# Kernel tuning notes

Measured on AMD Instinct MI355X. Metric: run time of the kernel, lower is better.

Reference implementation:

```python
import jax, jax.numpy as jnp
import numpy as np

EPS = 1e-5


def sage_conv(x, src, dst, Wl, Wr, b, n):
    # PyG SAGEConv: out_i = W_l * mean_{j in N(i)} x_j + W_r * x_i + b
    agg = jax.ops.segment_sum(x[src], dst, num_segments=n)  # [N, d]
    deg = jax.ops.segment_sum(jnp.ones_like(src, dtype=x.dtype), dst, num_segments=n)
    agg = agg / jnp.maximum(deg, 1.0)[:, None]
    return agg @ Wl + x @ Wr + b


def setup_inputs() -> dict:
    key = jax.random.key(0)
    ks = jax.random.split(key, 12)
    N, E, D_IN, D_H, D_OUT = 50000, 600000, 128, 128, 64
    x = jax.random.normal(ks[0], (N, D_IN), dtype=jnp.float32)
    edge_index = jax.random.randint(ks[1], (2, E), 0, N, dtype=jnp.int64)
    s_in = 1.0 / np.sqrt(D_IN)
    s_h = 1.0 / np.sqrt(D_H)
    return {
        "x": x,
        "edge_index": edge_index,
        "Wl0": jax.random.normal(ks[2], (D_IN, D_H), jnp.float32) * s_in,
        "Wr0": jax.random.normal(ks[3], (D_IN, D_H), jnp.float32) * s_in,
        "b0": jnp.zeros((D_H,), jnp.float32),
        "Wl1": jax.random.normal(ks[4], (D_H, D_H), jnp.float32) * s_h,
        "Wr1": jax.random.normal(ks[5], (D_H, D_H), jnp.float32) * s_h,
        "b1": jnp.zeros((D_H,), jnp.float32),
        "Wl2": jax.random.normal(ks[6], (D_H, D_OUT), jnp.float32) * s_h,
        "Wr2": jax.random.normal(ks[7], (D_H, D_OUT), jnp.float32) * s_h,
        "b2": jnp.zeros((D_OUT,), jnp.float32),
        "gamma": jnp.ones((D_H,), jnp.float32),
        "beta": jnp.zeros((D_H,), jnp.float32),
    }


def reference(x, edge_index, Wl0, Wr0, b0, Wl1, Wr1, b1, Wl2, Wr2, b2, gamma, beta):
    n = x.shape[0]
    src, dst = edge_index[0], edge_index[1]
    residual = x  # in_channels == hidden_channels -> no residual_transform
    # layer 0: conv + relu (+ dropout as identity in eval)
    h = jax.nn.relu(sage_conv(x, src, dst, Wl0, Wr0, b0, n))
    # middle layer: conv + BN(batch stats) + relu + residual
    h = sage_conv(h, src, dst, Wl1, Wr1, b1, n)
    mu = jnp.mean(h, axis=0)
    var = jnp.var(h, axis=0)  # biased, as in torch BN normalization
    h = (h - mu) * jax.lax.rsqrt(var + EPS) * gamma + beta
    h = jax.nn.relu(h) + residual
    # output layer
    h = sage_conv(h, src, dst, Wl2, Wr2, b2, n)
    return jax.nn.log_softmax(h, axis=-1)
```

## Files before the change

### kernel.cpp

```cpp
#include <hip/hip_runtime.h>
#include <hip/hip_bf16.h>


#define WS_EPS 1e-5f

typedef unsigned short ushort_t;
typedef unsigned int uint_t;
typedef unsigned char uchar_t;
typedef ushort_t ushort8 __attribute__((ext_vector_type(8)));
typedef short short8 __attribute__((ext_vector_type(8)));
typedef float f32x4 __attribute__((ext_vector_type(4)));
typedef _Float16 half2v __attribute__((ext_vector_type(2)));

__device__ __forceinline__ float bf2f(ushort_t u) {
    return __uint_as_float(((uint_t)u) << 16);
}
__device__ __forceinline__ ushort_t f2bf(float f) {
    uint_t u = __float_as_uint(f);
    u = (u + 0x7fffu + ((u >> 16) & 1u)) >> 16;
    return (ushort_t)u;
}
__device__ __forceinline__ uchar_t f2e4m3(float f) {
    _Float16 hf = (_Float16)f;
    uint_t h = (uint_t)__builtin_bit_cast(unsigned short, hf);
    uint_t s = (h >> 8) & 0x80u;
    uint_t r = h & 0x7fffu;
    if (r < 0x2400u) return (uchar_t)0;
    if (r > 0x5F40u) r = 0x5F00u;
    uint_t u = r - 0x2000u;
    uint_t m = (u + 0x3fu + ((u >> 7) & 1u)) >> 7;
    return (uchar_t)(s | m);
}

constexpr int SCHUNK = 4096;

__global__ __launch_bounds__(256) void k_scan_part(const int* __restrict__ deg,
                                                   int* __restrict__ bsum, int n) {
    int t = threadIdx.x;
    int base = blockIdx.x * SCHUNK + t * 16;
    int s = 0;
#pragma unroll
    for (int j = 0; j < 16; ++j) {
        int i = base + j;
        if (i < n) s += deg[i];
    }
#pragma unroll
    for (int d = 1; d < 64; d <<= 1) s += __shfl_xor(s, d);
    __shared__ int wt[4];
    if ((t & 63) == 0) wt[t >> 6] = s;
    __syncthreads();
    if (t == 0) bsum[blockIdx.x] = wt[0] + wt[1] + wt[2] + wt[3];
}

__global__ __launch_bounds__(64) void k_scan_bsum(const int* __restrict__ bsum,
                                                  int* __restrict__ boff,
                                                  int* __restrict__ off_n, int nb) {
    int lane = threadIdx.x;
    int carry = 0;
    for (int base = 0; base < nb; base += 64) {
        int t = base + lane;
        int v = (t < nb) ? bsum[t] : 0;
        int x = v;
#pragma unroll
        for (int d = 1; d < 64; d <<= 1) {
            int y = __shfl_up(x, d);
            if (lane >= d) x += y;
        }
        if (t < nb) boff[t] = carry + x - v;
        carry += __shfl(x, 63);
    }
    if (lane == 0) *off_n = carry;
}

__global__ __launch_bounds__(256) void k_scan_apply(const int* __restrict__ deg,
                                                    const int* __restrict__ boff,
                                                    int* __restrict__ off, int n) {
    int t = threadIdx.x;
    int lane = t & 63, wid = t >> 6;
    int base = blockIdx.x * SCHUNK + t * 16;
    int v[16];
    int s = 0;
#pragma unroll
    for (int j = 0; j < 16; ++j) {
        int i = base + j;
        v[j] = (i < n) ? deg[i] : 0;
        s += v[j];
    }
    int x = s;
#pragma unroll
    for (int d = 1; d < 64; d <<= 1) {
        int y = __shfl_up(x, d);
        if (lane >= d) x += y;
    }
    __shared__ int wtot[4];
    if (lane == 63) wtot[wid] = x;
    __syncthreads();
    int woff = 0;
    for (int wj = 0; wj < wid; ++wj) woff += wtot[wj];
    int run = boff[blockIdx.x] + woff + x - s;
#pragma unroll
    for (int j = 0; j < 16; ++j) {
        int i = base + j;
        if (i < n) off[i] = run;
        run += v[j];
    }
}

__global__ __launch_bounds__(256) void k_scatter(const int* __restrict__ ei,
                                                 const int* __restrict__ off,
                                                 int* __restrict__ cur,
                                                 int* __restrict__ csr, int E) {
    int e = blockIdx.x * 256 + threadIdx.x;
    if (e < E) {
        int d = ei[E + e];
        int s = ei[e];
        int p = atomicAdd(&cur[d], 1);
        csr[off[d] + p] = s;
    }
}

__global__ __launch_bounds__(256) void k_deg_prep(const int* __restrict__ ei,
                                                  int* __restrict__ deg, int E, int eb,
                                                  const float* __restrict__ x,
                                                  ushort_t* __restrict__ xb,
                                                  uchar_t* __restrict__ x8,
                                                  int total2, int nb_cvt,
                                                  const float* __restrict__ Wl0,
                                                  const float* __restrict__ Wr0,
                                                  const float* __restrict__ Wl1,
                                                  const float* __restrict__ Wr1,
                                                  const float* __restrict__ Wl2,
                                                  const float* __restrict__ Wr2,
                                                  ushort_t* __restrict__ wts) {
    int b = blockIdx.x;
    if (b < eb) {
        int e = b * 256 + threadIdx.x;
        if (e < E) atomicAdd(&deg[ei[E + e]], 1);
        return;
    }
    b -= eb;
    if (b < nb_cvt) {
        int i = b * 256 + threadIdx.x;
        if (i >= total2) return;
        float2 v = *(const float2*)&x[(size_t)i * 2];
        uint_t p = (uint_t)f2bf(v.x) | ((uint_t)f2bf(v.y) << 16);
        *(uint_t*)&xb[(size_t)i * 2] = p;
        ushort_t q = (ushort_t)((uint_t)f2e4m3(v.x) | ((uint_t)f2e4m3(v.y) << 8));
        *(ushort_t*)&x8[(size_t)i * 2] = q;
        return;
    }
    int id = (b - nb_cvt) * 256 + threadIdx.x;
    if (id >= 81920) return;
    const float* W;
    int rel, nout, base;
    if (id < 65536) {
        int m = id >> 14;
        rel = id & 16383;
        nout = 128;
        base = m << 14;
        W = (m == 0) ? Wl0 : (m == 1) ? Wr0 : (m == 2) ? Wl1 : Wr1;
    } else {
        int m = (id - 65536) >> 13;
        rel = (id - 65536) & 8191;
        nout = 64;
        base = 65536 + (m << 13);
        W = (m == 0) ? Wl2 : Wr2;
    }
    int c = rel >> 7;
    int k = rel & 127;
    wts[base + rel] = f2bf(W[(size_t)k * nout + c]);
}

template <int EPI>
__global__ __launch_bounds__(256, 4) void k_dgemm(const ushort_t* __restrict__ X1,
                                                  const ushort_t* __restrict__ W1,
                                                  const ushort_t* __restrict__ X2,
                                                  const ushort_t* __restrict__ W2,
                                                  const float* __restrict__ bias,
                                                  ushort_t* __restrict__ outp,
                                                  uchar_t* __restrict__ out8, int n) {
    constexpr int K = 128, NOUT = 128;
    __shared__ ushort_t Bs[2048 * 8];

    const int t = threadIdx.x;
    const int lane = t & 63;
    const int r16 = lane & 15, kb = lane >> 4;
    const int half = blockIdx.x & 1;
    const int colbase = half * 64;
    const int strip = (blockIdx.x >> 1) * 4 + (t >> 6);
    const int strips = (n + 15) >> 4;

    ushort8 wreg[8];
#pragma unroll
    for (int u = 0; u < 8; ++u) {
        int slot = u * 256 + t;
        int mat = slot >> 10;
        int rem = slot & 1023;
        int fnks = rem >> 6;
        int l = rem & 63;
        int fn = fnks >> 2, ks = fnks & 3;
        const ushort_t* Wm = mat ? W2 : W1;
        wreg[u] = *(const ushort8*)&Wm[(size_t)(colbase + fn * 16 + (l & 15)) * K +
                                       ks * 32 + (l >> 4) * 8];
    }
    const int arow = strip * 16 + r16;
    const bool rok = (arow < n);
    const size_t xo = (size_t)arow * K + kb * 8;
    short8 a1[4], a2[4];
#pragma unroll
    for (int ks = 0; ks < 4; ++ks)
        a1[ks] = rok ? *(const short8*)&X1[xo + ks * 32] : (short8)0;
#pragma unroll
    for (int ks = 0; ks < 4; ++ks)
        a2[ks] = rok ? *(const short8*)&X2[xo + ks * 32] : (short8)0;
#pragma unroll
    for (int u = 0; u < 8; ++u) {
        int slot = u * 256 + t;
        *(ushort8*)&Bs[(size_t)slot * 8] = wreg[u];
    }
    __syncthreads();

    f32x4 acc[4] = {(f32x4)0.f, (f32x4)0.f, (f32x4)0.f, (f32x4)0.f};
#pragma unroll
    for (int ks = 0; ks < 4; ++ks)
#pragma unroll
        for (int fn = 0; fn < 4; ++fn) {
            short8 b = *(const short8*)&Bs[((fn * 4 + ks) * 64 + lane) * 8];
            acc[fn] = __builtin_amdgcn_mfma_f32_16x16x32_bf16(a1[ks], b, acc[fn], 0, 0, 0);
        }
#pragma unroll
    for (int ks = 0; ks < 4; ++ks)
#pragma unroll
        for (int fn = 0; fn < 4; ++fn) {
            short8 b = *(const short8*)&Bs[((16 + fn * 4 + ks) * 64 + lane) * 8];
            acc[fn] = __builtin_amdgcn_mfma_f32_16x16x32_bf16(a2[ks], b, acc[fn], 0, 0, 0);
        }

    float bcol[4];
#pragma unroll
    for (int fn = 0; fn < 4; ++fn) bcol[fn] = bias[colbase + fn * 16 + r16];

    const int rb = strip * 16 + kb * 4;
#pragma unroll
    for (int r = 0; r < 4; ++r) {
        int row = rb + r;
        if (row >= n) continue;
#pragma unroll
        for (int fn = 0; fn < 4; ++fn) {
            int col = colbase + fn * 16 + r16;
            float v = acc[fn][r] + bcol[fn];
            if constexpr (EPI == 2) {
                v = fmaxf(v, 0.f);
                outp[(size_t)row * NOUT + col] = f2bf(v);
                out8[(size_t)row * NOUT + col] = f2e4m3(v);
            } else {
                outp[(size_t)row * NOUT + col] = f2bf(v);
            }
        }
    }
}

__global__ __launch_bounds__(256, 4) void k_cgemm(const ushort_t* __restrict__ H,
                                                  const ushort_t* __restrict__ WL,
                                                  const ushort_t* __restrict__ WR,
                                                  const float* __restrict__ b2,
                                                  ushort_t* __restrict__ A64,
                                                  ushort_t* __restrict__ Tb, int n) {
    constexpr int K = 128;
    __shared__ ushort_t Bs[2048 * 8];

    const int t = threadIdx.x;
    const int lane = t & 63;
    const int r16 = lane & 15, kb = lane >> 4;
    const int strip = blockIdx.x * 4 + (t >> 6);
    const int strips = (n + 15) >> 4;
    (void)strips;

    ushort8 wreg[8];
#pragma unroll
    for (int u = 0; u < 8; ++u) {
        int slot = u * 256 + t;
        int mat = slot >> 10;
        int rem = slot & 1023;
        int fnks = rem >> 6;
        int l = rem & 63;
        int fn = fnks >> 2, ks = fnks & 3;
        const ushort_t* Wm = mat ? WR : WL;
        wreg[u] = *(const ushort8*)&Wm[(size_t)(fn * 16 + (l & 15)) * K +
                                       ks * 32 + (l >> 4) * 8];
    }
    const int arow = strip * 16 + r16;
    const bool rok = (arow < n);
    const size_t xo = (size_t)arow * K + kb * 8;
    short8 a[4];
#pragma unroll
    for (int ks = 0; ks < 4; ++ks)
        a[ks] = rok ? *(const short8*)&H[xo + ks * 32] : (short8)0;
#pragma unroll
    for (int u = 0; u < 8; ++u) {
        int slot = u * 256 + t;
        *(ushort8*)&Bs[(size_t)slot * 8] = wreg[u];
    }
    __syncthreads();

    f32x4 aL[4] = {(f32x4)0.f, (f32x4)0.f, (f32x4)0.f, (f32x4)0.f};
    f32x4 aR[4] = {(f32x4)0.f, (f32x4)0.f, (f32x4)0.f, (f32x4)0.f};
#pragma unroll
    for (int ks = 0; ks < 4; ++ks)
#pragma unroll
        for (int fn = 0; fn < 4; ++fn) {
            short8 bl = *(const short8*)&Bs[((fn * 4 + ks) * 64 + lane) * 8];
            short8 br = *(const short8*)&Bs[((16 + fn * 4 + ks) * 64 + lane) * 8];
            aL[fn] = __builtin_amdgcn_mfma_f32_16x16x32_bf16(a[ks], bl, aL[fn], 0, 0, 0);
            aR[fn] = __builtin_amdgcn_mfma_f32_16x16x32_bf16(a[ks], br, aR[fn], 0, 0, 0);
        }

    float bcol[4];
#pragma unroll
    for (int fn = 0; fn < 4; ++fn) bcol[fn] = b2[fn * 16 + r16];

    const int rb = strip * 16 + kb * 4;
#pragma unroll
    for (int r = 0; r < 4; ++r) {
        int row = rb + r;
        if (row >= n) continue;
#pragma unroll
        for (int fn = 0; fn < 4; ++fn) {
            int col = fn * 16 + r16;
            A64[(size_t)row * 64 + col] = f2bf(aL[fn][r]);
            Tb[(size_t)row * 64 + col] = f2bf(aR[fn][r] + bcol[fn]);
        }
    }
}

__global__ __launch_bounds__(256) void k_bnstats(const ushort_t* __restrict__ P,
                                                 float* __restrict__ stats, int n) {
    int t = threadIdx.x;
    int c2 = t & 63;
    int h = t >> 6;
    int r0 = blockIdx.x * 64;
    int rend = min(r0 + 64, n);
    float s0 = 0.f, s1 = 0.f, q0 = 0.f, q1 = 0.f;
    for (int r = r0 + h; r < rend; r += 4) {
        uint_t pv = *(const uint_t*)&P[(size_t)r * 128 + c2 * 2];
        float p0 = __uint_as_float(pv << 16);
        float p1 = __uint_as_float(pv & 0xffff0000u);
        s0 += p0;
        q0 += p0 * p0;
        s1 += p1;
        q1 += p1 * p1;
    }
    __shared__ float sh[4][64][4];
    sh[h][c2][0] = s0;
    sh[h][c2][1] = s1;
    sh[h][c2][2] = q0;
    sh[h][c2][3] = q1;
    __syncthreads();
    if (h == 0) {
        float S0 = 0.f, S1 = 0.f, Q0 = 0.f, Q1 = 0.f;
#pragma unroll
        for (int j = 0; j < 4; ++j) {
            S0 += sh[j][c2][0];
            S1 += sh[j][c2][1];
            Q0 += sh[j][c2][2];
            Q1 += sh[j][c2][3];
        }
        atomicAdd(&stats[c2 * 2], S0);
        atomicAdd(&stats[c2 * 2 + 1], S1);
        atomicAdd(&stats[128 + c2 * 2], Q0);
        atomicAdd(&stats[128 + c2 * 2 + 1], Q1);
    }
}

__global__ __launch_bounds__(256) void k_segmean8(const uchar_t* __restrict__ U8,
                                                  const int* __restrict__ off,
                                                  const int* __restrict__ srcs,
                                                  ushort_t* __restrict__ out, int n) {
    int node = blockIdx.x * 32 + (threadIdx.x >> 3);
    int sub = threadIdx.x & 7;
    if (node >= n) return;
    int beg = off[node], end = off[node + 1];
    half2v aE0 = (half2v)0, aE1 = (half2v)0, aE2 = (half2v)0, aE3 = (half2v)0;
    half2v aO0 = (half2v)0, aO1 = (half2v)0, aO2 = (half2v)0, aO3 = (half2v)0;

#define DEC(dw, AE, AO)                                                           \
    {                                                                             \
        uint_t xe = (dw)&0x00ff00ffu;                                             \
        uint_t xo = ((dw) >> 8) & 0x00ff00ffu;                                    \
        uint_t he = ((xe & 0x00800080u) << 8) |                                   \
                    (((xe & 0x007f007fu) << 7) + 0x20002000u);                    \
        uint_t ho = ((xo & 0x00800080u) << 8) |                                   \
                    (((xo & 0x007f007fu) << 7) + 0x20002000u);                    \
        AE += __builtin_bit_cast(half2v, he);                                     \
        AO += __builtin_bit_cast(half2v, ho);                                     \
    }

    auto addrow = [&](int sidx) {
        uint4 v = *(const uint4*)&U8[(size_t)sidx * 128 + sub * 16];
        DEC(v.x, aE0, aO0)
        DEC(v.y, aE1, aO1)
        DEC(v.z, aE2, aO2)
        DEC(v.w, aE3, aO3)
    };
#undef DEC

    int i = beg;
    for (; i + 8 <= end; i += 8) {
        int sv[8];
#pragma unroll
        for (int u = 0; u < 8; ++u) sv[u] = srcs[i + u];
#pragma unroll
        for (int u = 0; u < 8; ++u) addrow(sv[u]);
    }
    for (; i < end; ++i) addrow(srcs[i]);

    int d = end - beg;
    float inv = 1.f / (float)(d > 1 ? d : 1);
    ushort8 o0, o1;
#define PACK(AE, AO, O, IDX)                     \
    O[IDX] = f2bf((float)AE[0] * inv);           \
    O[IDX + 1] = f2bf((float)AO[0] * inv);       \
    O[IDX + 2] = f2bf((float)AE[1] * inv);       \
    O[IDX + 3] = f2bf((float)AO[1] * inv);
    PACK(aE0, aO0, o0, 0)
    PACK(aE1, aO1, o0, 4)
    PACK(aE2, aO2, o1, 0)
    PACK(aE3, aO3, o1, 4)
#undef PACK
    *(ushort8*)&out[(size_t)node * 128 + sub * 16] = o0;
    *(ushort8*)&out[(size_t)node * 128 + sub * 16 + 8] = o1;
}

__global__ __launch_bounds__(256) void k_segmean_lsm(const ushort_t* __restrict__ A64,
                                                     const int* __restrict__ off,
                                                     const int* __restrict__ srcs,
                                                     const ushort_t* __restrict__ Tb,
                                                     float* __restrict__ out, int n) {
    int node = blockIdx.x * 32 + (threadIdx.x >> 3);
    int sub = threadIdx.x & 7;
    if (node >= n) return;
    int beg = off[node], end = off[node + 1];
    float a[8];
#pragma unroll
    for (int j = 0; j < 8; ++j) a[j] = 0.f;
    int i = beg;
    for (; i + 8 <= end; i += 8) {
        int sv[8];
#pragma unroll
        for (int u = 0; u < 8; ++u) sv[u] = srcs[i + u];
#pragma unroll
        for (int u = 0; u < 8; ++u) {
            ushort8 v = *(const ushort8*)&A64[(size_t)sv[u] * 64 + sub * 8];
#pragma unroll
            for (int j = 0; j < 8; ++j) a[j] += bf2f((ushort_t)v[j]);
        }
    }
    for (; i < end; ++i) {
        ushort8 v = *(const ushort8*)&A64[(size_t)srcs[i] * 64 + sub * 8];
#pragma unroll
        for (int j = 0; j < 8; ++j) a[j] += bf2f((ushort_t)v[j]);
    }
    int d = end - beg;
    float inv = 1.f / (float)(d > 1 ? d : 1);
    ushort8 tv = *(const ushort8*)&Tb[(size_t)node * 64 + sub * 8];
    float vv[8];
#pragma unroll
    for (int j = 0; j < 8; ++j) vv[j] = a[j] * inv + bf2f((ushort_t)tv[j]);
    float m = vv[0];
#pragma unroll
    for (int j = 1; j < 8; ++j) m = fmaxf(m, vv[j]);
#pragma unroll
    for (int dd = 1; dd < 8; dd <<= 1) m = fmaxf(m, __shfl_xor(m, dd));
    float e = 0.f;
#pragma unroll
    for (int j = 0; j < 8; ++j) e += expf(vv[j] - m);
#pragma unroll
    for (int dd = 1; dd < 8; dd <<= 1) e += __shfl_xor(e, dd);
    float lg = m + logf(e);
    f32x4 o0, o1;
#pragma unroll
    for (int j = 0; j < 4; ++j) {
        o0[j] = vv[j] - lg;
        o1[j] = vv[4 + j] - lg;
    }
    *(f32x4*)&out[(size_t)node * 64 + sub * 8] = o0;
    *(f32x4*)&out[(size_t)node * 64 + sub * 8 + 4] = o1;
}

__global__ __launch_bounds__(256) void k_bnapply(const ushort_t* __restrict__ P,
                                                 const ushort_t* __restrict__ Xb,
                                                 const float* __restrict__ stats,
                                                 const float* __restrict__ gamma,
                                                 const float* __restrict__ beta,
                                                 ushort_t* __restrict__ H, int n) {
    int i = blockIdx.x * 256 + threadIdx.x;
    if (i >= n * 64) return;
    int nd = i >> 6;
    int c = (i & 63) << 1;
    float inv_n = 1.f / (float)n;
    float mu0 = stats[c] * inv_n, mu1 = stats[c + 1] * inv_n;
    float v0 = stats[128 + c] * inv_n - mu0 * mu0;
    float v1 = stats[128 + c + 1] * inv_n - mu1 * mu1;
    float s0 = rsqrtf(v0 + WS_EPS) * gamma[c];
    float s1 = rsqrtf(v1 + WS_EPS) * gamma[c + 1];
    uint_t pv = *(const uint_t*)&P[(size_t)nd * 128 + c];
    uint_t xv = *(const uint_t*)&Xb[(size_t)nd * 128 + c];
    float p0 = __uint_as_float(pv << 16);
    float p1 = __uint_as_float(pv & 0xffff0000u);
    float x0 = __uint_as_float(xv << 16);
    float x1 = __uint_as_float(xv & 0xffff0000u);
    float h0 = fmaxf((p0 - mu0) * s0 + beta[c], 0.f) + x0;
    float h1 = fmaxf((p1 - mu1) * s1 + beta[c + 1], 0.f) + x1;
    uint_t pk = (uint_t)f2bf(h0) | ((uint_t)f2bf(h1) << 16);
    *(uint_t*)&H[(size_t)nd * 128 + c] = pk;
}

extern "C" void kernel_launch(void* const* d_in, const int* in_sizes, int n_in,
                              void* d_out, int out_size, void* d_ws, size_t ws_size,
                              hipStream_t stream) {
    const float* x     = (const float*)d_in[0];
    const int*   ei    = (const int*)d_in[1];
    const float* Wl0   = (const float*)d_in[2];
    const float* Wr0   = (const float*)d_in[3];
    const float* b0    = (const float*)d_in[4];
    const float* Wl1   = (const float*)d_in[5];
    const float* Wr1   = (const float*)d_in[6];
    const float* b1    = (const float*)d_in[7];
    const float* Wl2   = (const float*)d_in[8];
    const float* Wr2   = (const float*)d_in[9];
    const float* b2    = (const float*)d_in[10];
    const float* gamma = (const float*)d_in[11];
    const float* beta  = (const float*)d_in[12];

    const int n = in_sizes[0] / 128;
    const int E = in_sizes[1] / 2;
    const int nb_scan = (n + SCHUNK - 1) / SCHUNK;

    char* w = (char*)d_ws;
    auto alloc = [&](size_t bytes) -> void* {
        void* p = (void*)w;
        w += (bytes + 255) & ~(size_t)255;
        return p;
    };
    int*      deg   = (int*)alloc((size_t)n * 4);
    int*      cur   = (int*)alloc((size_t)n * 4);
    float*    stats = (float*)alloc(256 * 4);
    size_t    zbytes = (size_t)((char*)w - (char*)deg);
    int*      off   = (int*)alloc(((size_t)n + 1) * 4);
    int*      csr   = (int*)alloc((size_t)E * 4);
    int*      bsum  = (int*)alloc(256 * 4);
    int*      boff  = (int*)alloc(256 * 4);
    ushort_t* wts   = (ushort_t*)alloc((size_t)81920 * 2);
    ushort_t* xb    = (ushort_t*)alloc((size_t)n * 128 * 2);
    uchar_t*  x8    = (uchar_t*)alloc((size_t)n * 128);
    ushort_t* H     = (ushort_t*)alloc((size_t)n * 128 * 2);
    uchar_t*  H8    = (uchar_t*)alloc((size_t)n * 128);
    ushort_t* Pb    = (ushort_t*)alloc((size_t)n * 128 * 2);
    ushort_t* M     = (ushort_t*)alloc((size_t)n * 128 * 2);
    ushort_t* A64   = (ushort_t*)alloc((size_t)n * 64 * 2);
    ushort_t* Tb    = (ushort_t*)alloc((size_t)n * 64 * 2);

    ushort_t* WtL0 = wts;
    ushort_t* WtR0 = wts + 16384;
    ushort_t* WtL1 = wts + 32768;
    ushort_t* WtR1 = wts + 49152;
    ushort_t* WtL2 = wts + 65536;
    ushort_t* WtR2 = wts + 73728;

    hipMemsetAsync(deg, 0, zbytes, stream);

    const int eb = (E + 255) / 256;
    const int nb_cvt = (n * 64 + 255) / 256;
    k_deg_prep<<<eb + nb_cvt + 320, 256, 0, stream>>>(ei, deg, E, eb, x, xb, x8,
                                                      n * 64, nb_cvt,
                                                      Wl0, Wr0, Wl1, Wr1, Wl2, Wr2, wts);
    k_scan_part<<<nb_scan, 256, 0, stream>>>(deg, bsum, n);
    k_scan_bsum<<<1, 64, 0, stream>>>(bsum, boff, off + n, nb_scan);
    k_scan_apply<<<nb_scan, 256, 0, stream>>>(deg, boff, off, n);
    k_scatter<<<(E + 255) / 256, 256, 0, stream>>>(ei, off, cur, csr, E);

    const int strips = (n + 15) / 16;
    const int gb_d = 2 * ((strips + 3) / 4);
    const int gb_c = (strips + 3) / 4;
    const int smb = (n + 31) / 32;

    k_segmean8<<<smb, 256, 0, stream>>>(x8, off, csr, M, n);
    k_dgemm<2><<<gb_d, 256, 0, stream>>>(xb, WtR0, M, WtL0, b0, H, H8, n);

    k_segmean8<<<smb, 256, 0, stream>>>(H8, off, csr, M, n);
    k_dgemm<1><<<gb_d, 256, 0, stream>>>(H, WtR1, M, WtL1, b1, Pb, nullptr, n);
    k_bnstats<<<(n + 63) / 64, 256, 0, stream>>>(Pb, stats, n);
    k_bnapply<<<(n * 64 + 255) / 256, 256, 0, stream>>>(Pb, xb, stats, gamma, beta, H, n);

    k_cgemm<<<gb_c, 256, 0, stream>>>(H, WtL2, WtR2, b2, A64, Tb, n);
    k_segmean_lsm<<<smb, 256, 0, stream>>>(A64, off, csr, Tb, (float*)d_out, n);
}
```

Measured before the change: 251.0 us.

## Fuse BN statistics into dgemm epilogue and process two strips per wave

The separate k_bnstats kernel is removed. Batch-norm sums and sums of squares are now accumulated in the layer-1 GEMM epilogue with shuffles, shared-memory atomics and one global atomic per column per block. Each wave also computes two 16-row strips, which halves the grid and amortises the per-block weight load into shared memory. The stats use unrounded fp32 values rather than the re-read bf16 values. The wider per-wave tiles raise register pressure, and launch bounds drop from 4 to 3 blocks per CU.

Result: faster. 224.9 us (-10.4%).

```diff
diff --git a/kernel.cpp b/kernel.cpp
--- a/kernel.cpp
+++ b/kernel.cpp
@@ -172,23 +172,28 @@
 }
 
 template <int EPI>
-__global__ __launch_bounds__(256, 4) void k_dgemm(const ushort_t* __restrict__ X1,
+__global__ __launch_bounds__(256, 3) void k_dgemm(const ushort_t* __restrict__ X1,
                                                   const ushort_t* __restrict__ W1,
                                                   const ushort_t* __restrict__ X2,
                                                   const ushort_t* __restrict__ W2,
                                                   const float* __restrict__ bias,
                                                   ushort_t* __restrict__ outp,
-                                                  uchar_t* __restrict__ out8, int n) {
+                                                  uchar_t* __restrict__ out8,
+                                                  float* __restrict__ stats, int n) {
     constexpr int K = 128, NOUT = 128;
     __shared__ ushort_t Bs[2048 * 8];
+    __shared__ float sred[256];
 
     const int t = threadIdx.x;
     const int lane = t & 63;
     const int r16 = lane & 15, kb = lane >> 4;
     const int half = blockIdx.x & 1;
     const int colbase = half * 64;
-    const int strip = (blockIdx.x >> 1) * 4 + (t >> 6);
-    const int strips = (n + 15) >> 4;
+    const int w = t >> 6;
+    const int sA = (blockIdx.x >> 1) * 8 + w * 2;
+    const int sB = sA + 1;
+
+    if (EPI == 1) sred[t] = 0.f;
 
     ushort8 wreg[8];
 #pragma unroll
@@ -203,16 +208,23 @@
         wreg[u] = *(const ushort8*)&Wm[(size_t)(colbase + fn * 16 + (l & 15)) * K +
                                        ks * 32 + (l >> 4) * 8];
     }
-    const int arow = strip * 16 + r16;
-    const bool rok = (arow < n);
-    const size_t xo = (size_t)arow * K + kb * 8;
-    short8 a1[4], a2[4];
-#pragma unroll
-    for (int ks = 0; ks < 4; ++ks)
-        a1[ks] = rok ? *(const short8*)&X1[xo + ks * 32] : (short8)0;
-#pragma unroll
-    for (int ks = 0; ks < 4; ++ks)
-        a2[ks] = rok ? *(const short8*)&X2[xo + ks * 32] : (short8)0;
+    const int rowA = sA * 16 + r16, rowB = sB * 16 + r16;
+    const bool okA = rowA < n, okB = rowB < n;
+    const size_t xoA = (size_t)rowA * K + kb * 8;
+    const size_t xoB = (size_t)rowB * K + kb * 8;
+    short8 a1A[4], a2A[4], a1B[4], a2B[4];
+#pragma unroll
+    for (int ks = 0; ks < 4; ++ks)
+        a1A[ks] = okA ? *(const short8*)&X1[xoA + ks * 32] : (short8)0;
+#pragma unroll
+    for (int ks = 0; ks < 4; ++ks)
+        a2A[ks] = okA ? *(const short8*)&X2[xoA + ks * 32] : (short8)0;
+#pragma unroll
+    for (int ks = 0; ks < 4; ++ks)
+        a1B[ks] = okB ? *(const short8*)&X1[xoB + ks * 32] : (short8)0;
+#pragma unroll
+    for (int ks = 0; ks < 4; ++ks)
+        a2B[ks] = okB ? *(const short8*)&X2[xoB + ks * 32] : (short8)0;
 #pragma unroll
     for (int u = 0; u < 8; ++u) {
         int slot = u * 256 + t;
@@ -220,43 +232,94 @@
     }
     __syncthreads();
 
-    f32x4 acc[4] = {(f32x4)0.f, (f32x4)0.f, (f32x4)0.f, (f32x4)0.f};
+    f32x4 accA[4] = {(f32x4)0.f, (f32x4)0.f, (f32x4)0.f, (f32x4)0.f};
+    f32x4 accB[4] = {(f32x4)0.f, (f32x4)0.f, (f32x4)0.f, (f32x4)0.f};
 #pragma unroll
     for (int ks = 0; ks < 4; ++ks)
 #pragma unroll
         for (int fn = 0; fn < 4; ++fn) {
             short8 b = *(const short8*)&Bs[((fn * 4 + ks) * 64 + lane) * 8];
-            acc[fn] = __builtin_amdgcn_mfma_f32_16x16x32_bf16(a1[ks], b, acc[fn], 0, 0, 0);
+            accA[fn] = __builtin_amdgcn_mfma_f32_16x16x32_bf16(a1A[ks], b, accA[fn], 0, 0, 0);
+            accB[fn] = __builtin_amdgcn_mfma_f32_16x16x32_bf16(a1B[ks], b, accB[fn], 0, 0, 0);
         }
 #pragma unroll
     for (int ks = 0; ks < 4; ++ks)
 #pragma unroll
         for (int fn = 0; fn < 4; ++fn) {
             short8 b = *(const short8*)&Bs[((16 + fn * 4 + ks) * 64 + lane) * 8];
-            acc[fn] = __builtin_amdgcn_mfma_f32_16x16x32_bf16(a2[ks], b, acc[fn], 0, 0, 0);
+            accA[fn] = __builtin_amdgcn_mfma_f32_16x16x32_bf16(a2A[ks], b, accA[fn], 0, 0, 0);
+            accB[fn] = __builtin_amdgcn_mfma_f32_16x16x32_bf16(a2B[ks], b, accB[fn], 0, 0, 0);
         }
 
     float bcol[4];
 #pragma unroll
     for (int fn = 0; fn < 4; ++fn) bcol[fn] = bias[colbase + fn * 16 + r16];
 
-    const int rb = strip * 16 + kb * 4;
-#pragma unroll
-    for (int r = 0; r < 4; ++r) {
-        int row = rb + r;
-        if (row >= n) continue;
+    float ssum[4] = {0.f, 0.f, 0.f, 0.f}, qsum[4] = {0.f, 0.f, 0.f, 0.f};
+
+    {
+        const int rb = sA * 16 + kb * 4;
+#pragma unroll
+        for (int r = 0; r < 4; ++r) {
+            int row = rb + r;
+            if (row >= n) continue;
+#pragma unroll
+            for (int fn = 0; fn < 4; ++fn) {
+                int col = colbase + fn * 16 + r16;
+                float v = accA[fn][r] + bcol[fn];
+                if constexpr (EPI == 2) {
+                    v = fmaxf(v, 0.f);
+                    outp[(size_t)row * NOUT + col] = f2bf(v);
+                    out8[(size_t)row * NOUT + col] = f2e4m3(v);
+                } else {
+                    outp[(size_t)row * NOUT + col] = f2bf(v);
+                    ssum[fn] += v;
+                    qsum[fn] += v * v;
+                }
+            }
+        }
+    }
+    {
+        const int rb = sB * 16 + kb * 4;
+#pragma unroll
+        for (int r = 0; r < 4; ++r) {
+            int row = rb + r;
+            if (row >= n) continue;
+#pragma unroll
+            for (int fn = 0; fn < 4; ++fn) {
+                int col = colbase + fn * 16 + r16;
+                float v = accB[fn][r] + bcol[fn];
+                if constexpr (EPI == 2) {
+                    v = fmaxf(v, 0.f);
+                    outp[(size_t)row * NOUT + col] = f2bf(v);
+                    out8[(size_t)row * NOUT + col] = f2e4m3(v);
+                } else {
+                    outp[(size_t)row * NOUT + col] = f2bf(v);
+                    ssum[fn] += v;
+                    qsum[fn] += v * v;
+                }
+            }
+        }
+    }
+
+    if constexpr (EPI == 1) {
 #pragma unroll
         for (int fn = 0; fn < 4; ++fn) {
-            int col = colbase + fn * 16 + r16;
-            float v = acc[fn][r] + bcol[fn];
-            if constexpr (EPI == 2) {
-                v = fmaxf(v, 0.f);
-                outp[(size_t)row * NOUT + col] = f2bf(v);
-                out8[(size_t)row * NOUT + col] = f2e4m3(v);
-            } else {
-                outp[(size_t)row * NOUT + col] = f2bf(v);
+            ssum[fn] += __shfl_xor(ssum[fn], 16);
+            ssum[fn] += __shfl_xor(ssum[fn], 32);
+            qsum[fn] += __shfl_xor(qsum[fn], 16);
+            qsum[fn] += __shfl_xor(qsum[fn], 32);
+        }
+        if (kb == 0) {
+#pragma unroll
+            for (int fn = 0; fn < 4; ++fn) {
+                int col = colbase + fn * 16 + r16;
+                atomicAdd(&sred[col], ssum[fn]);
+                atomicAdd(&sred[128 + col], qsum[fn]);
             }
         }
+        __syncthreads();
+        atomicAdd(&stats[t], sred[t]);
     }
 }
 
@@ -273,8 +336,6 @@
     const int lane = t & 63;
     const int r16 = lane & 15, kb = lane >> 4;
     const int strip = blockIdx.x * 4 + (t >> 6);
-    const int strips = (n + 15) >> 4;
-    (void)strips;
 
     ushort8 wreg[8];
 #pragma unroll
@@ -330,45 +391,6 @@
             A64[(size_t)row * 64 + col] = f2bf(aL[fn][r]);
             Tb[(size_t)row * 64 + col] = f2bf(aR[fn][r] + bcol[fn]);
         }
-    }
-}
-
-__global__ __launch_bounds__(256) void k_bnstats(const ushort_t* __restrict__ P,
-                                                 float* __restrict__ stats, int n) {
-    int t = threadIdx.x;
-    int c2 = t & 63;
-    int h = t >> 6;
-    int r0 = blockIdx.x * 64;
-    int rend = min(r0 + 64, n);
-    float s0 = 0.f, s1 = 0.f, q0 = 0.f, q1 = 0.f;
-    for (int r = r0 + h; r < rend; r += 4) {
-        uint_t pv = *(const uint_t*)&P[(size_t)r * 128 + c2 * 2];
-        float p0 = __uint_as_float(pv << 16);
-        float p1 = __uint_as_float(pv & 0xffff0000u);
-        s0 += p0;
-        q0 += p0 * p0;
-        s1 += p1;
-        q1 += p1 * p1;
-    }
-    __shared__ float sh[4][64][4];
-    sh[h][c2][0] = s0;
-    sh[h][c2][1] = s1;
-    sh[h][c2][2] = q0;
-    sh[h][c2][3] = q1;
-    __syncthreads();
-    if (h == 0) {
-        float S0 = 0.f, S1 = 0.f, Q0 = 0.f, Q1 = 0.f;
-#pragma unroll
-        for (int j = 0; j < 4; ++j) {
-            S0 += sh[j][c2][0];
-            S1 += sh[j][c2][1];
-            Q0 += sh[j][c2][2];
-            Q1 += sh[j][c2][3];
-        }
-        atomicAdd(&stats[c2 * 2], S0);
-        atomicAdd(&stats[c2 * 2 + 1], S1);
-        atomicAdd(&stats[128 + c2 * 2], Q0);
-        atomicAdd(&stats[128 + c2 * 2 + 1], Q1);
     }
 }
 
@@ -580,16 +602,15 @@
     k_scatter<<<(E + 255) / 256, 256, 0, stream>>>(ei, off, cur, csr, E);
 
     const int strips = (n + 15) / 16;
-    const int gb_d = 2 * ((strips + 3) / 4);
+    const int gb_d = 2 * ((strips + 7) / 8);
     const int gb_c = (strips + 3) / 4;
     const int smb = (n + 31) / 32;
 
     k_segmean8<<<smb, 256, 0, stream>>>(x8, off, csr, M, n);
-    k_dgemm<2><<<gb_d, 256, 0, stream>>>(xb, WtR0, M, WtL0, b0, H, H8, n);
+    k_dgemm<2><<<gb_d, 256, 0, stream>>>(xb, WtR0, M, WtL0, b0, H, H8, nullptr, n);
 
     k_segmean8<<<smb, 256, 0, stream>>>(H8, off, csr, M, n);
-    k_dgemm<1><<<gb_d, 256, 0, stream>>>(H, WtR1, M, WtL1, b1, Pb, nullptr, n);
-    k_bnstats<<<(n + 63) / 64, 256, 0, stream>>>(Pb, stats, n);
+    k_dgemm<1><<<gb_d, 256, 0, stream>>>(H, WtR1, M, WtL1, b1, Pb, nullptr, stats, n);
     k_bnapply<<<(n * 64 + 255) / 256, 256, 0, stream>>>(Pb, xb, stats, gamma, beta, H, n);
 
     k_cgemm<<<gb_c, 256, 0, stream>>>(H, WtL2, WtR2, b2, A64, Tb, n);
```
